# Performance work log

Measured on AMD Instinct MI355X. Metric: run time of the kernel, lower is better.

Reference implementation:

```python
import jax, jax.numpy as jnp
import numpy as np


def setup_inputs() -> dict:
    key = jax.random.key(0)
    k1, k2, k3, k4 = jax.random.split(key, 4)
    N, D, B = 300000, 256, 512
    x = jax.random.normal(k1, (N, D), dtype=jnp.float32)
    batch = jnp.sort(jax.random.randint(k2, (N,), 0, B, dtype=jnp.int64))
    W1 = jax.random.normal(k3, (D, D // 2), dtype=jnp.float32) / np.sqrt(D)
    b1 = jnp.zeros((D // 2,), dtype=jnp.float32)
    W2 = jax.random.normal(k4, (D // 2, 1), dtype=jnp.float32) / np.sqrt(D // 2)
    b2 = jnp.zeros((1,), dtype=jnp.float32)
    return {"x": x, "batch": batch, "num_segments": B,
            "W1": W1, "b1": b1, "W2": W2, "b2": b2}


def reference(x, batch, num_segments, W1, b1, W2, b2):
    # attention MLP: Linear -> ReLU -> Linear, output [N, 1]
    h = jax.nn.relu(x @ W1 + b1)
    scores = h @ W2 + b2                       # [N, 1]
    # softmax over ALL nodes (dim=0), as in the original module
    w = jax.nn.softmax(scores, axis=0)          # [N, 1]
    # weighted segment-sum per graph; empty segments yield zero rows
    pooled = jax.ops.segment_sum(x * w, batch, num_segments=num_segments)
    return pooled                                # [num_segments, D]
```

## Files before the change

kernel.cpp:

```cpp
#include <hip/hip_runtime.h>
#include <hip/hip_fp16.h>
#include <math.h>

typedef __attribute__((ext_vector_type(8))) _Float16 f16x8;
typedef __attribute__((ext_vector_type(2))) __fp16 fp16x2;
typedef __attribute__((ext_vector_type(4))) float f32x4;

constexpr int D = 256;
constexpr int H = 128;
constexpr int KSTEPS = D / 32;
constexpr int BM = 64;

union FragH { uint4 u; f16x8 f; };
union H2U { fp16x2 h; unsigned int u; };

__device__ __forceinline__ unsigned int pkrtz(float a, float b) {
  H2U r; r.h = __builtin_amdgcn_cvt_pkrtz(a, b); return r.u;
}

__device__ __forceinline__ void gload16(const void* g, void* l) {
  __builtin_amdgcn_global_load_lds(
      (const __attribute__((address_space(1))) unsigned int*)g,
      (__attribute__((address_space(3))) unsigned int*)l, 16, 0, 0);
}
__device__ __forceinline__ void block_sync() {
  asm volatile("" ::: "memory");
  __builtin_amdgcn_s_barrier();
  asm volatile("" ::: "memory");
}

extern "C" __global__ void __launch_bounds__(256)
k_init(float* __restrict__ out, int out_size, float* __restrict__ zacc)
{
  const int i = blockIdx.x * 256 + threadIdx.x;
  if (i < out_size) out[i] = 0.0f;
  if (i == 0) *zacc = 0.0f;
}

extern "C" __global__ void __launch_bounds__(256)
k_pack(const float* __restrict__ W1, uint4* __restrict__ pw)
{
  const int g = blockIdx.x * 256 + threadIdx.x;
  const int c = g >> 9, ht = (g >> 6) & 7, l = g & 63;
  const int kbase = c * 32 + (l >> 4) * 8;
  const int col = ht * 16 + (l & 15);
  unsigned short q[8];
#pragma unroll
  for (int i = 0; i < 8; ++i) {
    const float v = W1[(size_t)(kbase + i) * H + col];
    const __half hh = __float2half(v);
    q[i] = __half_as_ushort(hh);
  }
  uint4 h4;
  h4.x = (unsigned)q[0] | ((unsigned)q[1] << 16);
  h4.y = (unsigned)q[2] | ((unsigned)q[3] << 16);
  h4.z = (unsigned)q[4] | ((unsigned)q[5] << 16);
  h4.w = (unsigned)q[6] | ((unsigned)q[7] << 16);
  pw[g] = h4;
}

extern "C" __global__ void __launch_bounds__(256, 6)
k_fused(const float* __restrict__ x, const int* __restrict__ batch,
        const uint4* __restrict__ pw, const float* __restrict__ b1,
        const float* __restrict__ W2, const float* __restrict__ b2,
        float* __restrict__ out, float* __restrict__ zacc, int N)
{
  __shared__ float4 xplane[2][512];
  __shared__ float sred[2][BM];
  __shared__ float wlds[BM];

  const int t = threadIdx.x;
  const int l = t & 63;
  const int w = t >> 6;
  const int lg = l >> 4;
  const int lr = l & 15;
  const int rg = w >> 1;
  const int cg = w & 1;
  const int n0 = blockIdx.x * BM;

  const char* xb = (const char*)x;

  auto STAGE = [&](int buf, int c) {
#pragma unroll
    for (int i = 0; i < 2; ++i) {
      const int plane = i * 4 + w;
      const int g = plane >> 1, p = plane & 1;
      const int srow = min(n0 + g * 16 + lr, N - 1);
      gload16(xb + (size_t)srow * 1024 + c * 128 + lg * 32 + p * 16,
              (char*)&xplane[buf][plane * 64 + l]);
    }
  };

  f32x4 acc[2][4] = {};

  STAGE(0, 0);
#pragma unroll 1
  for (int c = 0; c < KSTEPS; ++c) {
    const int cur = c & 1;
    FragH bw[4];
#pragma unroll
    for (int h = 0; h < 4; ++h)
      bw[h].u = pw[(c * 8 + cg * 4 + h) * 64 + l];
    if (c + 1 < KSTEPS) {
      STAGE(cur ^ 1, c + 1);
      asm volatile("s_waitcnt vmcnt(2)" ::: "memory");
    } else {
      asm volatile("s_waitcnt vmcnt(0)" ::: "memory");
    }
    block_sync();

#pragma unroll
    for (int s = 0; s < 2; ++s) {
      const int g = rg * 2 + s;
      const float4 u0 = xplane[cur][(g * 2 + 0) * 64 + l];
      const float4 u1 = xplane[cur][(g * 2 + 1) * 64 + l];
      FragH a;
      a.u.x = pkrtz(u0.x, u0.y);
      a.u.y = pkrtz(u0.z, u0.w);
      a.u.z = pkrtz(u1.x, u1.y);
      a.u.w = pkrtz(u1.z, u1.w);
#pragma unroll
      for (int h = 0; h < 4; ++h)
        acc[s][h] = __builtin_amdgcn_mfma_f32_16x16x32_f16(a.f, bw[h].f, acc[s][h], 0, 0, 0);
    }
    block_sync();
  }

  float bvv[4], wvv[4];
#pragma unroll
  for (int h = 0; h < 4; ++h) {
    const int col = (cg * 4 + h) * 16 + lr;
    bvv[h] = b1[col];
    wvv[h] = W2[col];
  }
#pragma unroll
  for (int s = 0; s < 2; ++s) {
#pragma unroll
    for (int r = 0; r < 4; ++r) {
      float p = 0.0f;
#pragma unroll
      for (int h = 0; h < 4; ++h)
        p = fmaf(fmaxf(acc[s][h][r] + bvv[h], 0.0f), wvv[h], p);
#pragma unroll
      for (int off = 1; off < 16; off <<= 1) p += __shfl_xor(p, off, 64);
      if (lr == 0) sred[cg][rg * 32 + s * 16 + lg * 4 + r] = p;
    }
  }
  __syncthreads();
  if (cg == 0) {
    const int row = rg * 32 + (l & 31);
    const int node = n0 + row;
    const float sc = sred[0][row] + sred[1][row] + b2[0];
    const float wgt = (l < 32 && node < N) ? __expf(sc) : 0.0f;
    if (l < 32) wlds[row] = wgt;
    float zs = wgt;
#pragma unroll
    for (int off = 1; off < 64; off <<= 1) zs += __shfl_xor(zs, off, 64);
    if (l == 0) atomicAdd(zacc, zs);
  }
  __syncthreads();

  {
    const int nStart = n0 + w * 16;
    const int nEnd = min(nStart + 16, N);
    if (nStart < nEnd) {
      float4 a4 = make_float4(0.f, 0.f, 0.f, 0.f);
      int bprev = batch[nStart];
      for (int n = nStart; n < nEnd; ++n) {
        const int b = batch[n];
        if (b != bprev) {
          float* o = out + (size_t)bprev * D + l * 4;
          atomicAdd(o + 0, a4.x); atomicAdd(o + 1, a4.y);
          atomicAdd(o + 2, a4.z); atomicAdd(o + 3, a4.w);
          a4 = make_float4(0.f, 0.f, 0.f, 0.f);
          bprev = b;
        }
        const float wgt = wlds[n - n0];
        const float4 xv = *reinterpret_cast<const float4*>(x + (size_t)n * D + l * 4);
        a4.x = fmaf(xv.x, wgt, a4.x);
        a4.y = fmaf(xv.y, wgt, a4.y);
        a4.z = fmaf(xv.z, wgt, a4.z);
        a4.w = fmaf(xv.w, wgt, a4.w);
      }
      float* o = out + (size_t)bprev * D + l * 4;
      atomicAdd(o + 0, a4.x); atomicAdd(o + 1, a4.y);
      atomicAdd(o + 2, a4.z); atomicAdd(o + 3, a4.w);
    }
  }
}

extern "C" __global__ void __launch_bounds__(256)
k_finish(float* __restrict__ out, const float* __restrict__ zacc, int size)
{
  const int i = blockIdx.x * 256 + threadIdx.x;
  if (i < size) out[i] *= (1.0f / *zacc);
}

extern "C" void kernel_launch(void* const* d_in, const int* in_sizes, int n_in,
                              void* d_out, int out_size, void* d_ws, size_t ws_size,
                              hipStream_t stream)
{
  const float* x     = (const float*)d_in[0];
  const int*   batch = (const int*)d_in[1];
  const float* W1 = (const float*)d_in[3];
  const float* b1 = (const float*)d_in[4];
  const float* W2 = (const float*)d_in[5];
  const float* b2 = (const float*)d_in[6];
  const int N = in_sizes[1];

  float* zacc = (float*)d_ws;
  uint4* pw   = (uint4*)((char*)d_ws + 256);

  k_init<<<(out_size + 255) / 256, 256, 0, stream>>>((float*)d_out, out_size, zacc);
  k_pack<<<16, 256, 0, stream>>>(W1, pw);

  const int g1 = (N + BM - 1) / BM;
  k_fused<<<g1, 256, 0, stream>>>(x, batch, pw, b1, W2, b2,
                                  (float*)d_out, zacc, N);

  k_finish<<<(out_size + 255) / 256, 256, 0, stream>>>((float*)d_out, zacc, out_size);
}
```

Before: 210.6 us.

## Stage whole 32-row x tile in LDS once with swizzle, drop per-k barriers

```diff
diff --git a/kernel.cpp b/kernel.cpp
--- a/kernel.cpp
+++ b/kernel.cpp
@@ -9,7 +9,7 @@
 constexpr int D = 256;
 constexpr int H = 128;
 constexpr int KSTEPS = D / 32;
-constexpr int BM = 64;
+constexpr int BM = 32;
 
 union FragH { uint4 u; f16x8 f; };
 union H2U { fp16x2 h; unsigned int u; };
@@ -59,13 +59,13 @@
   pw[g] = h4;
 }
 
-extern "C" __global__ void __launch_bounds__(256, 6)
+extern "C" __global__ void __launch_bounds__(256, 4)
 k_fused(const float* __restrict__ x, const int* __restrict__ batch,
         const uint4* __restrict__ pw, const float* __restrict__ b1,
         const float* __restrict__ W2, const float* __restrict__ b2,
         float* __restrict__ out, float* __restrict__ zacc, int N)
 {
-  __shared__ float4 xplane[2][512];
+  __shared__ float4 xtile4[BM * 64];
   __shared__ float sred[2][BM];
   __shared__ float wlds[BM];
 
@@ -79,51 +79,53 @@
   const int n0 = blockIdx.x * BM;
 
   const char* xb = (const char*)x;
-
-  auto STAGE = [&](int buf, int c) {
-#pragma unroll
-    for (int i = 0; i < 2; ++i) {
-      const int plane = i * 4 + w;
-      const int g = plane >> 1, p = plane & 1;
-      const int srow = min(n0 + g * 16 + lr, N - 1);
-      gload16(xb + (size_t)srow * 1024 + c * 128 + lg * 32 + p * 16,
-              (char*)&xplane[buf][plane * 64 + l]);
+  char* xt = (char*)xtile4;
+
+  FragH bw[4], nbw[4];
+#pragma unroll
+  for (int h = 0; h < 4; ++h)
+    bw[h].u = pw[(cg * 4 + h) * 64 + l];
+
+#pragma unroll
+  for (int i = 0; i < 8; ++i) {
+    const int row = w * 8 + i;
+    const int srow = min(n0 + row, N - 1);
+    const int sch = l ^ (row & 7);
+    gload16(xb + (size_t)srow * 1024 + sch * 16, xt + row * 1024 + l * 16);
+  }
+  asm volatile("s_waitcnt vmcnt(0)" ::: "memory");
+  block_sync();
+
+  const int arow = rg * 16 + lr;
+  const char* arb = xt + arow * 1024;
+  const int rx = (arow & 7);
+  f32x4 acc[4] = {};
+
+  float4 a0 = *(const float4*)(arb + ((lg * 2 + 0) ^ rx) * 16);
+  float4 a1 = *(const float4*)(arb + ((lg * 2 + 1) ^ rx) * 16);
+
+#pragma unroll
+  for (int c = 0; c < KSTEPS; ++c) {
+    float4 na0, na1;
+    if (c + 1 < KSTEPS) {
+      const int ch0 = (c + 1) * 8 + lg * 2;
+      na0 = *(const float4*)(arb + ((ch0 + 0) ^ rx) * 16);
+      na1 = *(const float4*)(arb + ((ch0 + 1) ^ rx) * 16);
+#pragma unroll
+      for (int h = 0; h < 4; ++h)
+        nbw[h].u = pw[((c + 1) * 8 + cg * 4 + h) * 64 + l];
     }
-  };
-
-  f32x4 acc[2][4] = {};
-
-  STAGE(0, 0);
-#pragma unroll 1
-  for (int c = 0; c < KSTEPS; ++c) {
-    const int cur = c & 1;
-    FragH bw[4];
+    FragH a;
+    a.u.x = pkrtz(a0.x, a0.y);
+    a.u.y = pkrtz(a0.z, a0.w);
+    a.u.z = pkrtz(a1.x, a1.y);
+    a.u.w = pkrtz(a1.z, a1.w);
 #pragma unroll
     for (int h = 0; h < 4; ++h)
-      bw[h].u = pw[(c * 8 + cg * 4 + h) * 64 + l];
-    if (c + 1 < KSTEPS) {
-      STAGE(cur ^ 1, c + 1);
-      asm volatile("s_waitcnt vmcnt(2)" ::: "memory");
-    } else {
-      asm volatile("s_waitcnt vmcnt(0)" ::: "memory");
-    }
-    block_sync();
-
-#pragma unroll
-    for (int s = 0; s < 2; ++s) {
-      const int g = rg * 2 + s;
-      const float4 u0 = xplane[cur][(g * 2 + 0) * 64 + l];
-      const float4 u1 = xplane[cur][(g * 2 + 1) * 64 + l];
-      FragH a;
-      a.u.x = pkrtz(u0.x, u0.y);
-      a.u.y = pkrtz(u0.z, u0.w);
-      a.u.z = pkrtz(u1.x, u1.y);
-      a.u.w = pkrtz(u1.z, u1.w);
-#pragma unroll
-      for (int h = 0; h < 4; ++h)
-        acc[s][h] = __builtin_amdgcn_mfma_f32_16x16x32_f16(a.f, bw[h].f, acc[s][h], 0, 0, 0);
-    }
-    block_sync();
+      acc[h] = __builtin_amdgcn_mfma_f32_16x16x32_f16(a.f, bw[h].f, acc[h], 0, 0, 0);
+#pragma unroll
+    for (int h = 0; h < 4; ++h) bw[h] = nbw[h];
+    a0 = na0; a1 = na1;
   }
 
   float bvv[4], wvv[4];
@@ -134,24 +136,20 @@
     wvv[h] = W2[col];
   }
 #pragma unroll
-  for (int s = 0; s < 2; ++s) {
-#pragma unroll
-    for (int r = 0; r < 4; ++r) {
-      float p = 0.0f;
-#pragma unroll
-      for (int h = 0; h < 4; ++h)
-        p = fmaf(fmaxf(acc[s][h][r] + bvv[h], 0.0f), wvv[h], p);
-#pragma unroll
-      for (int off = 1; off < 16; off <<= 1) p += __shfl_xor(p, off, 64);
-      if (lr == 0) sred[cg][rg * 32 + s * 16 + lg * 4 + r] = p;
-    }
+  for (int r = 0; r < 4; ++r) {
+    float p = 0.0f;
+#pragma unroll
+    for (int h = 0; h < 4; ++h)
+      p = fmaf(fmaxf(acc[h][r] + bvv[h], 0.0f), wvv[h], p);
+#pragma unroll
+    for (int off = 1; off < 16; off <<= 1) p += __shfl_xor(p, off, 64);
+    if (lr == 0) sred[cg][rg * 16 + lg * 4 + r] = p;
   }
   __syncthreads();
-  if (cg == 0) {
-    const int row = rg * 32 + (l & 31);
-    const int node = n0 + row;
+  if (w == 0) {
+    const int row = l & 31;
     const float sc = sred[0][row] + sred[1][row] + b2[0];
-    const float wgt = (l < 32 && node < N) ? __expf(sc) : 0.0f;
+    const float wgt = (l < 32) ? __expf(sc) : 0.0f;
     if (l < 32) wlds[row] = wgt;
     float zs = wgt;
 #pragma unroll
@@ -161,31 +159,29 @@
   __syncthreads();
 
   {
-    const int nStart = n0 + w * 16;
-    const int nEnd = min(nStart + 16, N);
-    if (nStart < nEnd) {
-      float4 a4 = make_float4(0.f, 0.f, 0.f, 0.f);
-      int bprev = batch[nStart];
-      for (int n = nStart; n < nEnd; ++n) {
-        const int b = batch[n];
-        if (b != bprev) {
-          float* o = out + (size_t)bprev * D + l * 4;
-          atomicAdd(o + 0, a4.x); atomicAdd(o + 1, a4.y);
-          atomicAdd(o + 2, a4.z); atomicAdd(o + 3, a4.w);
-          a4 = make_float4(0.f, 0.f, 0.f, 0.f);
-          bprev = b;
-        }
-        const float wgt = wlds[n - n0];
-        const float4 xv = *reinterpret_cast<const float4*>(x + (size_t)n * D + l * 4);
-        a4.x = fmaf(xv.x, wgt, a4.x);
-        a4.y = fmaf(xv.y, wgt, a4.y);
-        a4.z = fmaf(xv.z, wgt, a4.z);
-        a4.w = fmaf(xv.w, wgt, a4.w);
+    const int nStart = n0 + w * 8;
+    float4 a4 = make_float4(0.f, 0.f, 0.f, 0.f);
+    int bprev = batch[nStart];
+#pragma unroll 1
+    for (int n = nStart; n < nStart + 8; ++n) {
+      const int b = batch[n];
+      if (b != bprev) {
+        float* o = out + (size_t)bprev * D + l * 4;
+        atomicAdd(o + 0, a4.x); atomicAdd(o + 1, a4.y);
+        atomicAdd(o + 2, a4.z); atomicAdd(o + 3, a4.w);
+        a4 = make_float4(0.f, 0.f, 0.f, 0.f);
+        bprev = b;
       }
-      float* o = out + (size_t)bprev * D + l * 4;
-      atomicAdd(o + 0, a4.x); atomicAdd(o + 1, a4.y);
-      atomicAdd(o + 2, a4.z); atomicAdd(o + 3, a4.w);
+      const float wgt = wlds[n - n0];
+      const float4 xv = *reinterpret_cast<const float4*>(x + (size_t)n * D + l * 4);
+      a4.x = fmaf(xv.x, wgt, a4.x);
+      a4.y = fmaf(xv.y, wgt, a4.y);
+      a4.z = fmaf(xv.z, wgt, a4.z);
+      a4.w = fmaf(xv.w, wgt, a4.w);
     }
+    float* o = out + (size_t)bprev * D + l * 4;
+    atomicAdd(o + 0, a4.x); atomicAdd(o + 1, a4.y);
+    atomicAdd(o + 2, a4.z); atomicAdd(o + 3, a4.w);
   }
 }
 
```

Result: slower. 229.9 us (+9.2%).

## Give each wave its own rows with a barrier-free, triple-buffered x pipeline

Applied to the files above, without the earlier changes.

```diff
diff --git a/kernel.cpp b/kernel.cpp
--- a/kernel.cpp
+++ b/kernel.cpp
@@ -17,16 +17,10 @@
 __device__ __forceinline__ unsigned int pkrtz(float a, float b) {
   H2U r; r.h = __builtin_amdgcn_cvt_pkrtz(a, b); return r.u;
 }
-
 __device__ __forceinline__ void gload16(const void* g, void* l) {
   __builtin_amdgcn_global_load_lds(
       (const __attribute__((address_space(1))) unsigned int*)g,
       (__attribute__((address_space(3))) unsigned int*)l, 16, 0, 0);
-}
-__device__ __forceinline__ void block_sync() {
-  asm volatile("" ::: "memory");
-  __builtin_amdgcn_s_barrier();
-  asm volatile("" ::: "memory");
 }
 
 extern "C" __global__ void __launch_bounds__(256)
@@ -59,14 +53,13 @@
   pw[g] = h4;
 }
 
-extern "C" __global__ void __launch_bounds__(256, 6)
+extern "C" __global__ void __launch_bounds__(256, 4)
 k_fused(const float* __restrict__ x, const int* __restrict__ batch,
         const uint4* __restrict__ pw, const float* __restrict__ b1,
         const float* __restrict__ W2, const float* __restrict__ b2,
         float* __restrict__ out, float* __restrict__ zacc, int N)
 {
-  __shared__ float4 xplane[2][512];
-  __shared__ float sred[2][BM];
+  __shared__ char xlds[4 * 3 * 2048];
   __shared__ float wlds[BM];
 
   const int t = threadIdx.x;
@@ -74,86 +67,86 @@
   const int w = t >> 6;
   const int lg = l >> 4;
   const int lr = l & 15;
-  const int rg = w >> 1;
-  const int cg = w & 1;
   const int n0 = blockIdx.x * BM;
 
   const char* xb = (const char*)x;
 
-  auto STAGE = [&](int buf, int c) {
-#pragma unroll
-    for (int i = 0; i < 2; ++i) {
-      const int plane = i * 4 + w;
-      const int g = plane >> 1, p = plane & 1;
-      const int srow = min(n0 + g * 16 + lr, N - 1);
-      gload16(xb + (size_t)srow * 1024 + c * 128 + lg * 32 + p * 16,
-              (char*)&xplane[buf][plane * 64 + l]);
-    }
-  };
-
-  f32x4 acc[2][4] = {};
-
-  STAGE(0, 0);
-#pragma unroll 1
-  for (int c = 0; c < KSTEPS; ++c) {
-    const int cur = c & 1;
-    FragH bw[4];
-#pragma unroll
-    for (int h = 0; h < 4; ++h)
-      bw[h].u = pw[(c * 8 + cg * 4 + h) * 64 + l];
-    if (c + 1 < KSTEPS) {
-      STAGE(cur ^ 1, c + 1);
-      asm volatile("s_waitcnt vmcnt(2)" ::: "memory");
-    } else {
-      asm volatile("s_waitcnt vmcnt(0)" ::: "memory");
-    }
-    block_sync();
-
-#pragma unroll
-    for (int s = 0; s < 2; ++s) {
-      const int g = rg * 2 + s;
-      const float4 u0 = xplane[cur][(g * 2 + 0) * 64 + l];
-      const float4 u1 = xplane[cur][(g * 2 + 1) * 64 + l];
-      FragH a;
-      a.u.x = pkrtz(u0.x, u0.y);
-      a.u.y = pkrtz(u0.z, u0.w);
-      a.u.z = pkrtz(u1.x, u1.y);
-      a.u.w = pkrtz(u1.z, u1.w);
-#pragma unroll
-      for (int h = 0; h < 4; ++h)
-        acc[s][h] = __builtin_amdgcn_mfma_f32_16x16x32_f16(a.f, bw[h].f, acc[s][h], 0, 0, 0);
-    }
-    block_sync();
-  }
-
-  float bvv[4], wvv[4];
-#pragma unroll
-  for (int h = 0; h < 4; ++h) {
-    const int col = (cg * 4 + h) * 16 + lr;
+  float bvv[8], wvv[8];
+#pragma unroll
+  for (int h = 0; h < 8; ++h) {
+    const int col = h * 16 + lr;
     bvv[h] = b1[col];
     wvv[h] = W2[col];
   }
-#pragma unroll
-  for (int s = 0; s < 2; ++s) {
-#pragma unroll
-    for (int r = 0; r < 4; ++r) {
-      float p = 0.0f;
-#pragma unroll
-      for (int h = 0; h < 4; ++h)
-        p = fmaf(fmaxf(acc[s][h][r] + bvv[h], 0.0f), wvv[h], p);
-#pragma unroll
-      for (int off = 1; off < 16; off <<= 1) p += __shfl_xor(p, off, 64);
-      if (lr == 0) sred[cg][rg * 32 + s * 16 + lg * 4 + r] = p;
+  const float b2v = b2[0];
+  asm volatile("s_waitcnt vmcnt(0)" ::: "memory");
+
+  auto XSTAGE = [&](int c) {
+    char* dst = xlds + (w * 3 + (c % 3)) * 2048;
+#pragma unroll
+    for (int j = 0; j < 2; ++j) {
+      const int rl = j * 8 + (l >> 3);
+      const int srow = min(n0 + w * 16 + rl, N - 1);
+      const int sch = (l & 7) ^ (l >> 3);
+      gload16(xb + (size_t)srow * 1024 + c * 128 + sch * 16,
+              dst + j * 1024 + l * 16);
+    }
+  };
+
+  f32x4 acc[8] = {};
+  FragH bw[8];
+
+#pragma unroll
+  for (int h = 0; h < 8; ++h) bw[h].u = pw[h * 64 + l];
+  XSTAGE(0);
+  XSTAGE(1);
+
+#pragma unroll
+  for (int c = 0; c < KSTEPS; ++c) {
+    FragH nbw[8];
+    if (c + 1 < KSTEPS) {
+#pragma unroll
+      for (int h = 0; h < 8; ++h)
+        nbw[h].u = pw[((c + 1) * 8 + h) * 64 + l];
+      if (c + 2 < KSTEPS) XSTAGE(c + 2);
+    }
+    if (c < KSTEPS - 2)       asm volatile("s_waitcnt vmcnt(12)" ::: "memory");
+    else if (c == KSTEPS - 2) asm volatile("s_waitcnt vmcnt(10)" ::: "memory");
+    else                      asm volatile("s_waitcnt vmcnt(0)" ::: "memory");
+    __builtin_amdgcn_sched_barrier(0);
+
+    const char* buf = xlds + (w * 3 + (c % 3)) * 2048;
+    const float4 u0 = *(const float4*)(buf + lr * 128 + (((lg * 2 + 0) ^ (lr & 7)) * 16));
+    const float4 u1 = *(const float4*)(buf + lr * 128 + (((lg * 2 + 1) ^ (lr & 7)) * 16));
+    FragH a;
+    a.u.x = pkrtz(u0.x, u0.y);
+    a.u.y = pkrtz(u0.z, u0.w);
+    a.u.z = pkrtz(u1.x, u1.y);
+    a.u.w = pkrtz(u1.z, u1.w);
+#pragma unroll
+    for (int h = 0; h < 8; ++h)
+      acc[h] = __builtin_amdgcn_mfma_f32_16x16x32_f16(a.f, bw[h].f, acc[h], 0, 0, 0);
+#pragma unroll
+    for (int h = 0; h < 8; ++h) bw[h] = nbw[h];
+  }
+
+#pragma unroll
+  for (int r = 0; r < 4; ++r) {
+    float p = 0.0f;
+#pragma unroll
+    for (int h = 0; h < 8; ++h)
+      p = fmaf(fmaxf(acc[h][r] + bvv[h], 0.0f), wvv[h], p);
+#pragma unroll
+    for (int off = 1; off < 16; off <<= 1) p += __shfl_xor(p, off, 64);
+    if (lr == 0) {
+      const int row = w * 16 + lg * 4 + r;
+      const int node = n0 + row;
+      wlds[row] = (node < N) ? __expf(p + b2v) : 0.0f;
     }
   }
   __syncthreads();
-  if (cg == 0) {
-    const int row = rg * 32 + (l & 31);
-    const int node = n0 + row;
-    const float sc = sred[0][row] + sred[1][row] + b2[0];
-    const float wgt = (l < 32 && node < N) ? __expf(sc) : 0.0f;
-    if (l < 32) wlds[row] = wgt;
-    float zs = wgt;
+  if (w == 0) {
+    float zs = wlds[l];
 #pragma unroll
     for (int off = 1; off < 64; off <<= 1) zs += __shfl_xor(zs, off, 64);
     if (l == 0) atomicAdd(zacc, zs);
@@ -162,10 +155,11 @@
 
   {
     const int nStart = n0 + w * 16;
-    const int nEnd = min(nStart + 16, N);
-    if (nStart < nEnd) {
+    if (nStart < N) {
+      const int nEnd = min(nStart + 16, N);
       float4 a4 = make_float4(0.f, 0.f, 0.f, 0.f);
       int bprev = batch[nStart];
+#pragma unroll 1
       for (int n = nStart; n < nEnd; ++n) {
         const int b = batch[n];
         if (b != bprev) {
```

Measured after the change: 205.2 us. -2.5%, faster.
